# Optimization experiments

Measured on AMD Instinct MI355X. Metric: run time of the kernel, lower is better.

The kernel has to match this reference:

```python
import jax, jax.numpy as jnp
from jax import lax
import numpy as np

NA, NC = 3, 1
CONF_THRESH, IOU_THRESH = 0.5, 0.5


def _conv(x, w, b, pad):
    y = lax.conv_general_dilated(x, w, (1, 1), [(pad, pad), (pad, pad)],
                                 dimension_numbers=('NCHW', 'OIHW', 'NCHW'))
    return y + b[None, :, None, None]


def _maxpool2(x):
    return lax.reduce_window(x, -jnp.inf, lax.max, (1, 1, 2, 2), (1, 1, 2, 2), 'VALID')


def _stream(x, w1, b1, w2, b2):
    x = _maxpool2(jax.nn.relu(_conv(x, w1, b1, 1)))
    x = _maxpool2(jax.nn.relu(_conv(x, w2, b2, 1)))
    return x


def _pairwise_iou(b):
    # b: [N,4] in (x1,y1,x2,y2); matches torchvision box_iou (no area clamp)
    x1, y1, x2, y2 = b[:, 0], b[:, 1], b[:, 2], b[:, 3]
    area = (x2 - x1) * (y2 - y1)
    ix1 = jnp.maximum(x1[:, None], x1[None, :])
    iy1 = jnp.maximum(y1[:, None], y1[None, :])
    ix2 = jnp.minimum(x2[:, None], x2[None, :])
    iy2 = jnp.minimum(y2[:, None], y2[None, :])
    inter = jnp.clip(ix2 - ix1, 0.0) * jnp.clip(iy2 - iy1, 0.0)
    return inter / (area[:, None] + area[None, :] - inter)


def _nms_keep(boxes, scores, conf_keep, iou_thresh):
    # Greedy NMS over a fixed, small N; returns bool keep mask (conf + NMS).
    n = boxes.shape[0]
    order = jnp.argsort(-jnp.where(conf_keep, scores, -jnp.inf))
    iou = _pairwise_iou(boxes[order])  # [N,N] in score order
    idx = jnp.arange(n)

    def body(i, state):
        keep, suppressed = state
        valid = jnp.logical_not(suppressed[i])
        keep = keep.at[i].set(valid)
        suppressed = suppressed | (valid & (iou[i] > iou_thresh) & (idx > i))
        return keep, suppressed

    keep_sorted, _ = lax.fori_loop(0, n, body,
                                   (jnp.zeros(n, bool), jnp.zeros(n, bool)))
    keep = jnp.zeros(n, bool).at[order].set(keep_sorted)
    return keep & conf_keep


def setup_inputs() -> dict:
    key = jax.random.key(0)
    ks = jax.random.split(key, 14)
    s = 0.05
    inp = {
        'x': jax.random.normal(ks[0], (8, 3, 512, 512), jnp.float32),
        'rgb_w1': jax.random.normal(ks[1], (32, 3, 3, 3), jnp.float32) * s,
        'rgb_b1': jnp.zeros((32,), jnp.float32),
        'rgb_w2': jax.random.normal(ks[2], (64, 32, 3, 3), jnp.float32) * s,
        'rgb_b2': jnp.zeros((64,), jnp.float32),
        'ir_w1': jax.random.normal(ks[3], (32, 3, 3, 3), jnp.float32) * s,
        'ir_b1': jnp.zeros((32,), jnp.float32),
        'ir_w2': jax.random.normal(ks[4], (64, 32, 3, 3), jnp.float32) * s,
        'ir_b2': jnp.zeros((64,), jnp.float32),
        'fuse_w': jax.random.normal(ks[5], (128, 128, 3, 3), jnp.float32) * s,
        'fuse_b': jnp.zeros((128,), jnp.float32),
        'det_w': jax.random.normal(ks[6], (NA * (5 + NC), 128, 1, 1), jnp.float32),
        'det_b': jax.random.normal(ks[7], (NA * (5 + NC),), jnp.float32),
    }
    return inp


def reference(x, rgb_w1, rgb_b1, rgb_w2, rgb_b2,
              ir_w1, ir_b1, ir_w2, ir_b2,
              fuse_w, fuse_b, det_w, det_b):
    f1 = _stream(x, rgb_w1, rgb_b1, rgb_w2, rgb_b2)   # [B,64,H/4,W/4]
    f2 = _stream(x, ir_w1, ir_b1, ir_w2, ir_b2)       # [B,64,H/4,W/4]
    f = jnp.concatenate([f1, f2], axis=1)             # [B,128,H/4,W/4]
    f = jax.nn.relu(_conv(f, fuse_w, fuse_b, 1))
    f = jnp.mean(f, axis=(2, 3), keepdims=True)       # AdaptiveAvgPool2d((1,1))
    p = _conv(f, det_w, det_b, 0)                     # [B,18,1,1]
    B, C, H, W = p.shape
    p = p.reshape(B, NA, 5 + NC, H, W).transpose(0, 1, 3, 4, 2)  # [B,na,H,W,5+nc]
    boxes = p[..., :4].reshape(B, -1, 4)              # [B, na*H*W, 4]
    scores = jax.nn.sigmoid(p[..., 4]).reshape(B, -1) # [B, na*H*W]
    conf_keep = scores > CONF_THRESH
    keep = jax.vmap(_nms_keep, in_axes=(0, 0, 0, None))(boxes, scores, conf_keep,
                                                        IOU_THRESH)
    # Fixed-shape equivalent of the per-image variable-length preds list:
    # preds[b] == boxes[b][keep[b]].
    return p, boxes, scores, keep
```

## Files before the change

kernel.cpp:

```cpp
#include <hip/hip_runtime.h>
#include <math.h>


typedef __bf16 bf16x8 __attribute__((ext_vector_type(8)));
typedef float f32x4 __attribute__((ext_vector_type(4)));

static __device__ __forceinline__ ushort f2bf(float f) {
    unsigned u = __float_as_uint(f);
    unsigned r = (u + 0x7fffu + ((u >> 16) & 1u)) >> 16;
    return (ushort)r;
}
static __device__ __forceinline__ float bf2f(ushort h) {
    return __uint_as_float(((unsigned)h) << 16);
}
static __device__ __forceinline__ void gl_lds16(const void* g, void* l) {
    __builtin_amdgcn_global_load_lds(
        (const __attribute__((address_space(1))) void*)g,
        (__attribute__((address_space(3))) void*)l, 16, 0, 0);
}

__global__ __launch_bounds__(256) void w1prep(
    const float* __restrict__ w_rgb, const float* __restrict__ w_ir,
    uint* __restrict__ W1p)
{
    int i = blockIdx.x * 256 + threadIdx.x;
    if (i >= 2048) return;
    int s = i >> 10, r = i & 1023;
    int oc = r >> 5, k = r & 31;
    const float* w = s ? w_ir : w_rgb;
    float v = (k < 27) ? w[oc * 27 + k] : 0.f;
    ushort h = f2bf(v);
    W1p[i] = (uint)h | ((uint)f2bf(v - bf2f(h)) << 16);
}

__global__ __launch_bounds__(256) void conv1_mfma(
    const float* __restrict__ x, const uint* __restrict__ W1p,
    const float* __restrict__ bias, ushort* __restrict__ C1h,
    ushort* __restrict__ C1l)
{
    __shared__ uint S[3 * 4 * 132];
    __shared__ float pool[4][32][32];

    const int seg = blockIdx.x, Y = blockIdx.y, b = blockIdx.z;
    const int tid = threadIdx.x, wsub = tid >> 6, lane = tid & 63;
    const int n = lane & 15, q = lane >> 4;

    uint4 bu0a = *(const uint4*)&W1p[n * 32 + q * 8];
    uint4 bu0b = *(const uint4*)&W1p[n * 32 + q * 8 + 4];
    uint4 bu1a = *(const uint4*)&W1p[(16 + n) * 32 + q * 8];
    uint4 bu1b = *(const uint4*)&W1p[(16 + n) * 32 + q * 8 + 4];

    const int ih0 = 2 * Y - 1, iw0 = seg * 128 - 1;
    for (int i = tid; i < 1584; i += 256) {
        int c = i / 528, rem = i - c * 528;
        int r = rem / 132, cc = rem - r * 132;
        int ih = ih0 + r, iw = iw0 + cc;
        float v = 0.f;
        if (cc < 130 && ih >= 0 && ih < 512 && iw >= 0 && iw < 512)
            v = x[((b * 3 + c) * 512 + ih) * 512 + iw];
        ushort h = f2bf(v);
        S[i] = (uint)h | ((uint)f2bf(v - bf2f(h)) << 16);
    }

    uint4 bh0v, bl0v, bh1v, bl1v;
    {
        uint u0[8], u1[8];
        *(uint4*)&u0[0] = bu0a; *(uint4*)&u0[4] = bu0b;
        *(uint4*)&u1[0] = bu1a; *(uint4*)&u1[4] = bu1b;
        uint* bh0 = (uint*)&bh0v; uint* bl0 = (uint*)&bl0v;
        uint* bh1 = (uint*)&bh1v; uint* bl1 = (uint*)&bl1v;
#pragma unroll
        for (int j = 0; j < 4; ++j) {
            bh0[j] = (u0[2 * j] & 0xffffu) | (u0[2 * j + 1] << 16);
            bl0[j] = (u0[2 * j] >> 16) | (u0[2 * j + 1] & 0xffff0000u);
            bh1[j] = (u1[2 * j] & 0xffffu) | (u1[2 * j + 1] << 16);
            bl1[j] = (u1[2 * j] >> 16) | (u1[2 * j + 1] & 0xffff0000u);
        }
    }
    bf16x8 Bh0 = __builtin_bit_cast(bf16x8, bh0v);
    bf16x8 Bl0 = __builtin_bit_cast(bf16x8, bl0v);
    bf16x8 Bh1 = __builtin_bit_cast(bf16x8, bh1v);
    bf16x8 Bl1 = __builtin_bit_cast(bf16x8, bl1v);

    int idx[8];
    const int off0 = (wsub & 1) * 132 + (wsub >> 1) * 64 + n;
#pragma unroll
    for (int e = 0; e < 8; ++e) {
        int k = q * 8 + e;
        int c = (k >= 18) ? ((k >= 27) ? 3 : 2) : ((k >= 9) ? 1 : 0);
        int t = k - c * 9;
        int ky = (t >= 6) ? 2 : ((t >= 3) ? 1 : 0);
        int kx = t - ky * 3;
        idx[e] = (k < 27) ? ((c * 4 + ky) * 132 + kx + off0) : 0;
    }
    __syncthreads();

    f32x4 acc[4][2];
#pragma unroll
    for (int mt = 0; mt < 4; ++mt)
#pragma unroll
        for (int nt = 0; nt < 2; ++nt) acc[mt][nt] = (f32x4){0.f, 0.f, 0.f, 0.f};

#pragma unroll
    for (int mt = 0; mt < 4; ++mt) {
        uint u[8];
#pragma unroll
        for (int e = 0; e < 8; ++e) u[e] = S[idx[e] + mt * 16];
        uint4 ahv, alv;
        uint* ah = (uint*)&ahv;
        uint* al = (uint*)&alv;
#pragma unroll
        for (int j = 0; j < 4; ++j) {
            ah[j] = (u[2 * j] & 0xffffu) | (u[2 * j + 1] << 16);
            al[j] = (u[2 * j] >> 16) | (u[2 * j + 1] & 0xffff0000u);
        }
        bf16x8 Ah = __builtin_bit_cast(bf16x8, ahv);
        bf16x8 Al = __builtin_bit_cast(bf16x8, alv);
        __builtin_amdgcn_s_setprio(1);
        acc[mt][0] = __builtin_amdgcn_mfma_f32_16x16x32_bf16(Ah, Bh0, acc[mt][0], 0, 0, 0);
        acc[mt][1] = __builtin_amdgcn_mfma_f32_16x16x32_bf16(Ah, Bh1, acc[mt][1], 0, 0, 0);
        acc[mt][0] = __builtin_amdgcn_mfma_f32_16x16x32_bf16(Ah, Bl0, acc[mt][0], 0, 0, 0);
        acc[mt][1] = __builtin_amdgcn_mfma_f32_16x16x32_bf16(Ah, Bl1, acc[mt][1], 0, 0, 0);
        acc[mt][0] = __builtin_amdgcn_mfma_f32_16x16x32_bf16(Al, Bh0, acc[mt][0], 0, 0, 0);
        acc[mt][1] = __builtin_amdgcn_mfma_f32_16x16x32_bf16(Al, Bh1, acc[mt][1], 0, 0, 0);
        __builtin_amdgcn_s_setprio(0);
    }

#pragma unroll
    for (int mt = 0; mt < 4; ++mt)
#pragma unroll
        for (int nt = 0; nt < 2; ++nt) {
            int oc = nt * 16 + n;
            int plx = mt * 8 + q * 2;
            pool[wsub][plx][oc]     = fmaxf(acc[mt][nt][0], acc[mt][nt][1]);
            pool[wsub][plx + 1][oc] = fmaxf(acc[mt][nt][2], acc[mt][nt][3]);
        }
    __syncthreads();
    {
        int plx = tid >> 2, ocq = tid & 3;
        int wp = plx >> 5, pl = plx & 31;
        __attribute__((aligned(16))) ushort hb[8], lb[8];
#pragma unroll
        for (int e = 0; e < 8; ++e) {
            int oc = ocq * 8 + e;
            float v = fmaxf(pool[wp * 2][pl][oc], pool[wp * 2 + 1][pl][oc]);
            v = fmaxf(v + bias[oc], 0.f);
            ushort h = f2bf(v);
            hb[e] = h;
            lb[e] = f2bf(v - bf2f(h));
        }
        int ow = seg * 64 + plx;
        size_t base = (((size_t)((b * 256 + Y) * 256 + ow)) << 5) + ocq * 8;
        *(uint4*)(C1h + base) = *(const uint4*)hb;
        *(uint4*)(C1l + base) = *(const uint4*)lb;
    }
}

__global__ __launch_bounds__(256) void conv2_mfma(
    const ushort* __restrict__ C1h, const ushort* __restrict__ C1l,
    const float* __restrict__ w2, const float* __restrict__ bias,
    ushort* __restrict__ Ahi, ushort* __restrict__ Alo, int stream_base)
{
    __shared__ __attribute__((aligned(16))) char lds[58368];
    ushort* BhL = (ushort*)(lds + 33792);
    ushort* BlL = (ushort*)(lds + 46080);
    float (*pool)[32][64] = (float (*)[32][64])lds;

    const int seg = blockIdx.x, Y = blockIdx.y, b = blockIdx.z;
    const int tid = threadIdx.x, wsub = tid >> 6, lane = tid & 63;
    const int n = lane & 15, q = lane >> 4;
    const int rs = wsub & 1;
    const int xs = wsub >> 1;

    const uint4 zero4 = make_uint4(0u, 0u, 0u, 0u);

    f32x4 acc[4][4];
#pragma unroll
    for (int mt = 0; mt < 4; ++mt)
#pragma unroll
        for (int nt = 0; nt < 4; ++nt) acc[mt][nt] = (f32x4){0.f, 0.f, 0.f, 0.f};

    for (int ky = 0; ky < 3; ++ky) {
        if (ky) __syncthreads();

        {
            const int hl = wsub >> 1, rsS = wsub & 1;
            const int yy = 2 * Y + rsS + ky - 1;
            char* dstbase = lds + hl * 16896 + rsS * 8448 + 64;
            if (yy >= 0 && yy < 256) {
                const ushort* src = (hl ? C1l : C1h)
                    + ((size_t)(b * 256 + yy) * 256 + seg * 128) * 32;
                const char* s8 = (const char*)src + lane * 16;
#pragma unroll
                for (int j = 0; j < 8; ++j)
                    gl_lds16(s8 + j * 1024, dstbase + j * 1024);
            } else {
#pragma unroll
                for (int j = 0; j < 8; ++j)
                    *(uint4*)(dstbase + j * 1024 + lane * 16) = zero4;
            }
        }
        if (tid < 32) {
            int combo = tid >> 3;
            int hl = combo >> 1, rsE = combo & 1;
            int e = (tid >> 2) & 1, part = tid & 3;
            int yy = 2 * Y + rsE + ky - 1;
            int xp = seg * 128 + (e ? 128 : -1);
            uint4 v = zero4;
            if (yy >= 0 && yy < 256 && xp >= 0 && xp < 256) {
                const ushort* src = (hl ? C1l : C1h)
                    + ((size_t)(b * 256 + yy) * 256 + xp) * 32 + part * 8;
                v = *(const uint4*)src;
            }
            *(uint4*)(lds + hl * 16896 + rsE * 8448 + (e ? 129 * 64 : 0) + part * 16) = v;
        }
        for (int i = tid; i < 6144; i += 256) {
            int t = ky * 3 + (i >> 11), r = i & 2047;
            float v = w2[r * 9 + t];
            ushort h = f2bf(v);
            BhL[i] = h;
            BlL[i] = f2bf(v - bf2f(h));
        }
        __syncthreads();

        for (int kx = 0; kx < 3; ++kx) {
            uint4 cH[4], cL[4];
#pragma unroll
            for (int mt = 0; mt < 4; ++mt) {
                int off = rs * 8448 + (xs * 64 + mt * 16 + n + kx) * 64 + q * 16;
                cH[mt] = *(const uint4*)(lds + off);
                cL[mt] = *(const uint4*)(lds + 16896 + off);
            }
            bf16x8 bh[4], bl[4];
#pragma unroll
            for (int nt = 0; nt < 4; ++nt) {
                int off = kx * 2048 + (nt * 16 + n) * 32 + q * 8;
                bh[nt] = __builtin_bit_cast(bf16x8, *(const uint4*)&BhL[off]);
                bl[nt] = __builtin_bit_cast(bf16x8, *(const uint4*)&BlL[off]);
            }
            __builtin_amdgcn_s_setprio(1);
#pragma unroll
            for (int mt = 0; mt < 4; ++mt) {
                bf16x8 ah = __builtin_bit_cast(bf16x8, cH[mt]);
#pragma unroll
                for (int nt = 0; nt < 4; ++nt)
                    acc[mt][nt] = __builtin_amdgcn_mfma_f32_16x16x32_bf16(ah, bh[nt], acc[mt][nt], 0, 0, 0);
            }
#pragma unroll
            for (int mt = 0; mt < 4; ++mt) {
                bf16x8 ah = __builtin_bit_cast(bf16x8, cH[mt]);
#pragma unroll
                for (int nt = 0; nt < 4; ++nt)
                    acc[mt][nt] = __builtin_amdgcn_mfma_f32_16x16x32_bf16(ah, bl[nt], acc[mt][nt], 0, 0, 0);
            }
#pragma unroll
            for (int mt = 0; mt < 4; ++mt) {
                bf16x8 al = __builtin_bit_cast(bf16x8, cL[mt]);
#pragma unroll
                for (int nt = 0; nt < 4; ++nt)
                    acc[mt][nt] = __builtin_amdgcn_mfma_f32_16x16x32_bf16(al, bh[nt], acc[mt][nt], 0, 0, 0);
            }
            __builtin_amdgcn_s_setprio(0);
        }
    }

    __syncthreads();

#pragma unroll
    for (int mt = 0; mt < 4; ++mt)
#pragma unroll
        for (int nt = 0; nt < 4; ++nt) {
            int oc = nt * 16 + n;
            int plx = mt * 8 + q * 2;
            pool[wsub][plx][oc]     = fmaxf(acc[mt][nt][0], acc[mt][nt][1]);
            pool[wsub][plx + 1][oc] = fmaxf(acc[mt][nt][2], acc[mt][nt][3]);
        }
    __syncthreads();

    {
        int plx = tid >> 2, ocq = tid & 3;
        int wp = plx >> 5, pl = plx & 31;
        __attribute__((aligned(16))) ushort hb[16], lb[16];
#pragma unroll
        for (int e = 0; e < 16; ++e) {
            int oc = ocq * 16 + e;
            float v = fmaxf(pool[wp * 2][pl][oc], pool[wp * 2 + 1][pl][oc]);
            v = fmaxf(v + bias[oc], 0.f);
            ushort h = f2bf(v);
            hb[e] = h;
            lb[e] = f2bf(v - bf2f(h));
        }
        int gx = seg * 64 + plx;
        int cpl = (stream_base >> 5) + (ocq >> 1);
        int cho = (ocq & 1) * 16;
        size_t base = (((size_t)(((b * 4 + cpl) * 128 + Y) * 128 + gx)) << 5) + cho;
        uint4* dh = (uint4*)(Ahi + base);
        uint4* dl = (uint4*)(Alo + base);
        dh[0] = *(const uint4*)&hb[0];
        dh[1] = *(const uint4*)&hb[8];
        dl[0] = *(const uint4*)&lb[0];
        dl[1] = *(const uint4*)&lb[8];
    }
}

__global__ __launch_bounds__(256) void wprep(
    const float* __restrict__ fw, ushort* __restrict__ Whi,
    ushort* __restrict__ Wlo)
{
    int idx = blockIdx.x * 256 + threadIdx.x;
    if (idx >= 147456) return;
    int kk = idx & 31;
    int oc = (idx >> 5) & 127;
    int ct = idx >> 12;
    int c = ct / 9, t = ct - c * 9;
    int ic = c * 32 + kk;
    int ky = t / 3, kx = t - ky * 3;
    float v = fw[((oc * 128 + ic) * 3 + ky) * 3 + kx];
    ushort h = f2bf(v);
    Whi[idx] = h;
    Wlo[idx] = f2bf(v - bf2f(h));
}

__global__ __launch_bounds__(256, 2) void fuse_mfma(
    const ushort* __restrict__ Ahi, const ushort* __restrict__ Alo,
    const ushort* __restrict__ Whi, const ushort* __restrict__ Wlo,
    const float* __restrict__ bias, float* __restrict__ featsum)
{
    __shared__ float partial[4][128];
    const int b = blockIdx.x, ypair = blockIdx.y;
    const int tid = threadIdx.x, wsub = tid >> 6, lane = tid & 63;
    const int n = lane & 15, q = lane >> 4;
    const int y = ypair * 2 + (wsub >> 1);
    const int xbase = (wsub & 1) * 64;

    f32x4 acc[4][8];
#pragma unroll
    for (int mt = 0; mt < 4; ++mt)
#pragma unroll
        for (int g = 0; g < 8; ++g) acc[mt][g] = (f32x4){0.f, 0.f, 0.f, 0.f};

    const uint4 zero4 = make_uint4(0u, 0u, 0u, 0u);

    auto loadA = [&](int tc, uint4* oh, uint4* ol) {
        int c = tc / 9, t = tc - c * 9;
        int ky = t / 3, kx = t - ky * 3;
        int yy = y + ky - 1;
        bool yok = (yy >= 0) & (yy < 128);
#pragma unroll
        for (int mt = 0; mt < 4; ++mt) {
            int xp = xbase + mt * 16 + n + kx - 1;
            bool ok = yok & (xp >= 0) & (xp < 128);
            int yyc = ok ? yy : 0, xpc = ok ? xp : 0;
            size_t aoff = (((size_t)(((b * 4 + c) * 128 + yyc) * 128 + xpc)) << 5) + q * 8;
            oh[mt] = ok ? *(const uint4*)(Ahi + aoff) : zero4;
            ol[mt] = ok ? *(const uint4*)(Alo + aoff) : zero4;
        }
    };

    uint4 pAh[4], pAl[4];
    loadA(0, pAh, pAl);

    const ushort* WhiB = Whi + n * 32 + q * 8;
    const ushort* WloB = Wlo + n * 32 + q * 8;

    uint4 nBh[4], nBl[4];
#pragma unroll
    for (int j = 0; j < 4; ++j) {
        nBh[j] = *(const uint4*)(WhiB + j * 512);
        nBl[j] = *(const uint4*)(WloB + j * 512);
    }

    for (int tc = 0; tc < 36; ++tc) {
        uint4 cAh[4], cAl[4];
#pragma unroll
        for (int mt = 0; mt < 4; ++mt) { cAh[mt] = pAh[mt]; cAl[mt] = pAl[mt]; }
        if (tc + 1 < 36) loadA(tc + 1, pAh, pAl);
#pragma unroll
        for (int g = 0; g < 8; ++g) {
            const int slot = g & 3;
            bf16x8 bh = __builtin_bit_cast(bf16x8, nBh[slot]);
            bf16x8 bl = __builtin_bit_cast(bf16x8, nBl[slot]);
            {
                size_t off = (size_t)(tc * 8 + g + 4) * 512;
                nBh[slot] = *(const uint4*)(WhiB + off);
                nBl[slot] = *(const uint4*)(WloB + off);
            }
#pragma unroll
            for (int mt = 0; mt < 4; ++mt) {
                bf16x8 ah = __builtin_bit_cast(bf16x8, cAh[mt]);
                acc[mt][g] = __builtin_amdgcn_mfma_f32_16x16x32_bf16(ah, bh, acc[mt][g], 0, 0, 0);
            }
#pragma unroll
            for (int mt = 0; mt < 4; ++mt) {
                bf16x8 ah = __builtin_bit_cast(bf16x8, cAh[mt]);
                acc[mt][g] = __builtin_amdgcn_mfma_f32_16x16x32_bf16(ah, bl, acc[mt][g], 0, 0, 0);
            }
#pragma unroll
            for (int mt = 0; mt < 4; ++mt) {
                bf16x8 al = __builtin_bit_cast(bf16x8, cAl[mt]);
                acc[mt][g] = __builtin_amdgcn_mfma_f32_16x16x32_bf16(al, bh, acc[mt][g], 0, 0, 0);
            }
        }
    }

#pragma unroll
    for (int g = 0; g < 8; ++g) {
        float bv = bias[g * 16 + n];
        float v = 0.f;
#pragma unroll
        for (int mt = 0; mt < 4; ++mt)
#pragma unroll
            for (int r = 0; r < 4; ++r) v += fmaxf(acc[mt][g][r] + bv, 0.f);
        v += __shfl_xor(v, 16);
        v += __shfl_xor(v, 32);
        if (lane < 16) partial[wsub][g * 16 + lane] = v;
    }
    __syncthreads();
    if (tid < 128) {
        float v = partial[0][tid] + partial[1][tid] + partial[2][tid] + partial[3][tid];
        atomicAdd(&featsum[b * 128 + tid], v);
    }
}

__global__ void det_nms(const float* __restrict__ featsum,
                        const float* __restrict__ dw, const float* __restrict__ db,
                        float* __restrict__ out)
{
    const int b = threadIdx.x;
    if (b >= 8) return;
    const float inv = 1.0f / 16384.0f;

    float p[18];
    for (int j = 0; j < 18; ++j) {
        float a = db[j];
        const float* wp = &dw[j * 128];
        const float* f = &featsum[b * 128];
        for (int c = 0; c < 128; ++c) a = fmaf(wp[c], f[c] * inv, a);
        p[j] = a;
    }
    for (int a = 0; a < 3; ++a)
        for (int e = 0; e < 6; ++e) out[b * 18 + a * 6 + e] = p[a * 6 + e];

    float bx[3][4], sc[3];
    bool ck[3];
    for (int a = 0; a < 3; ++a) {
        for (int k = 0; k < 4; ++k) {
            bx[a][k] = p[a * 6 + k];
            out[144 + b * 12 + a * 4 + k] = bx[a][k];
        }
        float sg = 1.f / (1.f + expf(-p[a * 6 + 4]));
        sc[a] = sg;
        ck[a] = sg > 0.5f;
        out[240 + b * 3 + a] = sg;
    }

    float key[3];
    int order[3];
    bool used[3] = {false, false, false};
    for (int a = 0; a < 3; ++a) key[a] = ck[a] ? sc[a] : -INFINITY;
    for (int i = 0; i < 3; ++i) {
        int best = -1;
        float bk = 0.f;
        for (int a = 0; a < 3; ++a) {
            if (used[a]) continue;
            if (best < 0 || key[a] > bk) { best = a; bk = key[a]; }
        }
        order[i] = best;
        used[best] = true;
    }

    float X1[3], Y1[3], X2[3], Y2[3], AR[3];
    for (int i = 0; i < 3; ++i) {
        int o = order[i];
        X1[i] = bx[o][0]; Y1[i] = bx[o][1];
        X2[i] = bx[o][2]; Y2[i] = bx[o][3];
        AR[i] = (X2[i] - X1[i]) * (Y2[i] - Y1[i]);
    }
    bool suppressed[3] = {false, false, false}, keep_s[3];
    for (int i = 0; i < 3; ++i) {
        bool valid = !suppressed[i];
        keep_s[i] = valid;
        if (valid) {
            for (int j = i + 1; j < 3; ++j) {
                float ix1 = fmaxf(X1[i], X1[j]), iy1 = fmaxf(Y1[i], Y1[j]);
                float ix2 = fminf(X2[i], X2[j]), iy2 = fminf(Y2[i], Y2[j]);
                float inter = fmaxf(ix2 - ix1, 0.f) * fmaxf(iy2 - iy1, 0.f);
                float iou = inter / (AR[i] + AR[j] - inter);
                if (iou > 0.5f) suppressed[j] = true;
            }
        }
    }
    bool keep[3];
    for (int i = 0; i < 3; ++i) keep[order[i]] = keep_s[i];
    for (int a = 0; a < 3; ++a)
        out[264 + b * 3 + a] = (keep[a] && ck[a]) ? 1.f : 0.f;
}

__global__ void zero_feat(float* __restrict__ p)
{
    int i = blockIdx.x * 256 + threadIdx.x;
    if (i < 1024) p[i] = 0.f;
}

extern "C" void kernel_launch(void* const* d_in, const int* in_sizes, int n_in,
                              void* d_out, int out_size, void* d_ws, size_t ws_size,
                              hipStream_t stream)
{
    const float* x      = (const float*)d_in[0];
    const float* rgb_w1 = (const float*)d_in[1];
    const float* rgb_b1 = (const float*)d_in[2];
    const float* rgb_w2 = (const float*)d_in[3];
    const float* rgb_b2 = (const float*)d_in[4];
    const float* ir_w1  = (const float*)d_in[5];
    const float* ir_b1  = (const float*)d_in[6];
    const float* ir_w2  = (const float*)d_in[7];
    const float* ir_b2  = (const float*)d_in[8];
    const float* fuse_w = (const float*)d_in[9];
    const float* fuse_b = (const float*)d_in[10];
    const float* det_w  = (const float*)d_in[11];
    const float* det_b  = (const float*)d_in[12];
    float* out = (float*)d_out;

    char* ws = (char*)d_ws;
    ushort* C1h  = (ushort*)(ws);
    ushort* C1l  = (ushort*)(ws + 33554432);
    ushort* Whi  = (ushort*)(ws);
    ushort* Wlo  = (ushort*)(ws + 299008);
    float*  feat = (float*)(ws + 598016);
    ushort* Ahi  = (ushort*)(ws + 67108864);
    ushort* Alo  = (ushort*)(ws + 100663296);
    uint*   W1p  = (uint*)(ws + 134209536);

    dim3 blk(256);
    hipLaunchKernelGGL(w1prep, dim3(8), blk, 0, stream, rgb_w1, ir_w1, W1p);
    hipLaunchKernelGGL(conv1_mfma, dim3(4, 256, 8), blk, 0, stream, x, W1p, rgb_b1, C1h, C1l);
    hipLaunchKernelGGL(conv2_mfma, dim3(2, 128, 8), blk, 0, stream, C1h, C1l, rgb_w2, rgb_b2, Ahi, Alo, 0);
    hipLaunchKernelGGL(conv1_mfma, dim3(4, 256, 8), blk, 0, stream, x, W1p + 1024, ir_b1, C1h, C1l);
    hipLaunchKernelGGL(conv2_mfma, dim3(2, 128, 8), blk, 0, stream, C1h, C1l, ir_w2, ir_b2, Ahi, Alo, 64);
    hipLaunchKernelGGL(wprep, dim3(576), blk, 0, stream, fuse_w, Whi, Wlo);
    hipLaunchKernelGGL(zero_feat, dim3(4), blk, 0, stream, feat);
    hipLaunchKernelGGL(fuse_mfma, dim3(8, 64), blk, 0, stream, Ahi, Alo, Whi, Wlo, fuse_b, feat);
    hipLaunchKernelGGL(det_nms, dim3(1), dim3(64), 0, stream, feat, det_w, det_b, out);
}
```

Before: 494.8 us.

## Stage fuse-conv activations and weights in LDS; pad pool arrays against bank conflicts

The fuse convolution kernel now copies one input row (hi/lo bf16) and three kx weight slices per (channel chunk, ky) into LDS using global_load_lds, then reads both from LDS for all three kx taps. Previously each wave loaded A and B directly from global memory. The work is split so each block handles one output row, with waves divided across x-halves and output-channel halves, which doubles the grid. The pool scratch arrays in conv1 and conv2 also get one padding column to reduce LDS bank conflicts. In exchange, 64KB of LDS lowers occupancy and adds barriers each iteration.

```diff
diff --git a/kernel.cpp b/kernel.cpp
--- a/kernel.cpp
+++ b/kernel.cpp
@@ -39,7 +39,7 @@
     ushort* __restrict__ C1l)
 {
     __shared__ uint S[3 * 4 * 132];
-    __shared__ float pool[4][32][32];
+    __shared__ float pool[4][32][33];
 
     const int seg = blockIdx.x, Y = blockIdx.y, b = blockIdx.z;
     const int tid = threadIdx.x, wsub = tid >> 6, lane = tid & 63;
@@ -164,7 +164,7 @@
     __shared__ __attribute__((aligned(16))) char lds[58368];
     ushort* BhL = (ushort*)(lds + 33792);
     ushort* BlL = (ushort*)(lds + 46080);
-    float (*pool)[32][64] = (float (*)[32][64])lds;
+    float (*pool)[32][65] = (float (*)[32][65])lds;
 
     const int seg = blockIdx.x, Y = blockIdx.y, b = blockIdx.z;
     const int tid = threadIdx.x, wsub = tid >> 6, lane = tid & 63;
@@ -326,86 +326,106 @@
     const ushort* __restrict__ Whi, const ushort* __restrict__ Wlo,
     const float* __restrict__ bias, float* __restrict__ featsum)
 {
-    __shared__ float partial[4][128];
-    const int b = blockIdx.x, ypair = blockIdx.y;
+    __shared__ __attribute__((aligned(16))) char lds[65536];
+
+    const int b = blockIdx.x, y = blockIdx.y;
     const int tid = threadIdx.x, wsub = tid >> 6, lane = tid & 63;
     const int n = lane & 15, q = lane >> 4;
-    const int y = ypair * 2 + (wsub >> 1);
-    const int xbase = (wsub & 1) * 64;
-
-    f32x4 acc[4][8];
+    const int p = wsub & 1, o = wsub >> 1;
+
+    const uint4 zero4 = make_uint4(0u, 0u, 0u, 0u);
+    const bool badL = (p == 0) & (n == 0);
+    const bool badR = (p == 1) & (n == 15);
+
+    f32x4 acc[4][4];
 #pragma unroll
     for (int mt = 0; mt < 4; ++mt)
 #pragma unroll
-        for (int g = 0; g < 8; ++g) acc[mt][g] = (f32x4){0.f, 0.f, 0.f, 0.f};
-
-    const uint4 zero4 = make_uint4(0u, 0u, 0u, 0u);
-
-    auto loadA = [&](int tc, uint4* oh, uint4* ol) {
-        int c = tc / 9, t = tc - c * 9;
-        int ky = t / 3, kx = t - ky * 3;
-        int yy = y + ky - 1;
-        bool yok = (yy >= 0) & (yy < 128);
-#pragma unroll
-        for (int mt = 0; mt < 4; ++mt) {
-            int xp = xbase + mt * 16 + n + kx - 1;
-            bool ok = yok & (xp >= 0) & (xp < 128);
-            int yyc = ok ? yy : 0, xpc = ok ? xp : 0;
-            size_t aoff = (((size_t)(((b * 4 + c) * 128 + yyc) * 128 + xpc)) << 5) + q * 8;
-            oh[mt] = ok ? *(const uint4*)(Ahi + aoff) : zero4;
-            ol[mt] = ok ? *(const uint4*)(Alo + aoff) : zero4;
-        }
-    };
-
-    uint4 pAh[4], pAl[4];
-    loadA(0, pAh, pAl);
-
-    const ushort* WhiB = Whi + n * 32 + q * 8;
-    const ushort* WloB = Wlo + n * 32 + q * 8;
-
-    uint4 nBh[4], nBl[4];
-#pragma unroll
-    for (int j = 0; j < 4; ++j) {
-        nBh[j] = *(const uint4*)(WhiB + j * 512);
-        nBl[j] = *(const uint4*)(WloB + j * 512);
-    }
-
-    for (int tc = 0; tc < 36; ++tc) {
-        uint4 cAh[4], cAl[4];
-#pragma unroll
-        for (int mt = 0; mt < 4; ++mt) { cAh[mt] = pAh[mt]; cAl[mt] = pAl[mt]; }
-        if (tc + 1 < 36) loadA(tc + 1, pAh, pAl);
-#pragma unroll
-        for (int g = 0; g < 8; ++g) {
-            const int slot = g & 3;
-            bf16x8 bh = __builtin_bit_cast(bf16x8, nBh[slot]);
-            bf16x8 bl = __builtin_bit_cast(bf16x8, nBl[slot]);
-            {
-                size_t off = (size_t)(tc * 8 + g + 4) * 512;
-                nBh[slot] = *(const uint4*)(WhiB + off);
-                nBl[slot] = *(const uint4*)(WloB + off);
-            }
-#pragma unroll
-            for (int mt = 0; mt < 4; ++mt) {
-                bf16x8 ah = __builtin_bit_cast(bf16x8, cAh[mt]);
-                acc[mt][g] = __builtin_amdgcn_mfma_f32_16x16x32_bf16(ah, bh, acc[mt][g], 0, 0, 0);
-            }
-#pragma unroll
-            for (int mt = 0; mt < 4; ++mt) {
-                bf16x8 ah = __builtin_bit_cast(bf16x8, cAh[mt]);
-                acc[mt][g] = __builtin_amdgcn_mfma_f32_16x16x32_bf16(ah, bl, acc[mt][g], 0, 0, 0);
-            }
-#pragma unroll
-            for (int mt = 0; mt < 4; ++mt) {
-                bf16x8 al = __builtin_bit_cast(bf16x8, cAl[mt]);
-                acc[mt][g] = __builtin_amdgcn_mfma_f32_16x16x32_bf16(al, bh, acc[mt][g], 0, 0, 0);
-            }
-        }
-    }
-
-#pragma unroll
-    for (int g = 0; g < 8; ++g) {
-        float bv = bias[g * 16 + n];
+        for (int g = 0; g < 4; ++g) acc[mt][g] = (f32x4){0.f, 0.f, 0.f, 0.f};
+
+    for (int c = 0; c < 4; ++c) {
+        for (int ky = 0; ky < 3; ++ky) {
+            if (c | ky) __syncthreads();
+
+            if (wsub == 0) {
+                const int yy = y + ky - 1;
+                if (yy >= 0 && yy < 128) {
+                    const char* sH = (const char*)(Ahi + ((size_t)((b * 4 + c) * 128 + yy)) * 4096) + lane * 16;
+                    const char* sL = (const char*)(Alo + ((size_t)((b * 4 + c) * 128 + yy)) * 4096) + lane * 16;
+#pragma unroll
+                    for (int j = 0; j < 8; ++j) {
+                        gl_lds16(sH + j * 1024, lds + j * 1024);
+                        gl_lds16(sL + j * 1024, lds + 8192 + j * 1024);
+                    }
+                } else {
+#pragma unroll
+                    for (int j = 0; j < 16; ++j)
+                        *(uint4*)(lds + j * 1024 + lane * 16) = zero4;
+                }
+            } else {
+                const size_t woff = (size_t)(c * 9 + ky * 3) * 4096;
+                const int bc0 = (wsub - 1) * 16;
+#pragma unroll
+                for (int j = 0; j < 16; ++j) {
+                    int bc = bc0 + j;
+                    const ushort* base = (bc < 24) ? (Whi + woff) : (Wlo + woff);
+                    int co = (bc < 24) ? bc : (bc - 24);
+                    gl_lds16((const char*)base + co * 1024 + lane * 16,
+                             lds + 16384 + bc * 1024);
+                }
+            }
+            __syncthreads();
+
+#pragma unroll
+            for (int kx = 0; kx < 3; ++kx) {
+                bf16x8 bh[4], bl[4];
+#pragma unroll
+                for (int g = 0; g < 4; ++g) {
+                    int boff = 16384 + kx * 8192 + (o * 64 + g * 16 + n) * 64 + q * 16;
+                    bh[g] = __builtin_bit_cast(bf16x8, *(const uint4*)(lds + boff));
+                    bl[g] = __builtin_bit_cast(bf16x8, *(const uint4*)(lds + boff + 24576));
+                }
+                uint4 cH[4], cL[4];
+#pragma unroll
+                for (int mt = 0; mt < 4; ++mt) {
+                    int s = p * 64 + mt * 16 + n + kx - 1;
+                    if (kx == 0 && mt == 0) s = (s < 0) ? 0 : s;
+                    if (kx == 2 && mt == 3) s = (s > 127) ? 127 : s;
+                    int aoff = s * 64 + q * 16;
+                    cH[mt] = *(const uint4*)(lds + aoff);
+                    cL[mt] = *(const uint4*)(lds + 8192 + aoff);
+                }
+                if (kx == 0) { cH[0] = badL ? zero4 : cH[0]; cL[0] = badL ? zero4 : cL[0]; }
+                if (kx == 2) { cH[3] = badR ? zero4 : cH[3]; cL[3] = badR ? zero4 : cL[3]; }
+
+#pragma unroll
+                for (int g = 0; g < 4; ++g) {
+#pragma unroll
+                    for (int mt = 0; mt < 4; ++mt) {
+                        bf16x8 ah = __builtin_bit_cast(bf16x8, cH[mt]);
+                        acc[mt][g] = __builtin_amdgcn_mfma_f32_16x16x32_bf16(ah, bh[g], acc[mt][g], 0, 0, 0);
+                    }
+#pragma unroll
+                    for (int mt = 0; mt < 4; ++mt) {
+                        bf16x8 ah = __builtin_bit_cast(bf16x8, cH[mt]);
+                        acc[mt][g] = __builtin_amdgcn_mfma_f32_16x16x32_bf16(ah, bl[g], acc[mt][g], 0, 0, 0);
+                    }
+#pragma unroll
+                    for (int mt = 0; mt < 4; ++mt) {
+                        bf16x8 al = __builtin_bit_cast(bf16x8, cL[mt]);
+                        acc[mt][g] = __builtin_amdgcn_mfma_f32_16x16x32_bf16(al, bh[g], acc[mt][g], 0, 0, 0);
+                    }
+                }
+            }
+        }
+    }
+
+    __syncthreads();
+    float* partial = (float*)lds;
+
+#pragma unroll
+    for (int g = 0; g < 4; ++g) {
+        float bv = bias[o * 64 + g * 16 + n];
         float v = 0.f;
 #pragma unroll
         for (int mt = 0; mt < 4; ++mt)
@@ -413,13 +433,11 @@
             for (int r = 0; r < 4; ++r) v += fmaxf(acc[mt][g][r] + bv, 0.f);
         v += __shfl_xor(v, 16);
         v += __shfl_xor(v, 32);
-        if (lane < 16) partial[wsub][g * 16 + lane] = v;
+        if (lane < 16) partial[p * 128 + o * 64 + g * 16 + lane] = v;
     }
     __syncthreads();
-    if (tid < 128) {
-        float v = partial[0][tid] + partial[1][tid] + partial[2][tid] + partial[3][tid];
-        atomicAdd(&featsum[b * 128 + tid], v);
-    }
+    if (tid < 128)
+        atomicAdd(&featsum[b * 128 + tid], partial[tid] + partial[128 + tid]);
 }
 
 __global__ void det_nms(const float* __restrict__ featsum,
@@ -539,6 +557,6 @@
     hipLaunchKernelGGL(conv2_mfma, dim3(2, 128, 8), blk, 0, stream, C1h, C1l, ir_w2, ir_b2, Ahi, Alo, 64);
     hipLaunchKernelGGL(wprep, dim3(576), blk, 0, stream, fuse_w, Whi, Wlo);
     hipLaunchKernelGGL(zero_feat, dim3(4), blk, 0, stream, feat);
-    hipLaunchKernelGGL(fuse_mfma, dim3(8, 64), blk, 0, stream, Ahi, Alo, Whi, Wlo, fuse_b, feat);
+    hipLaunchKernelGGL(fuse_mfma, dim3(8, 128), blk, 0, stream, Ahi, Alo, Whi, Wlo, fuse_b, feat);
     hipLaunchKernelGGL(det_nms, dim3(1), dim3(64), 0, stream, feat, det_w, det_b, out);
 }
```

New measurement: 701.0 us. +41.7%, slower.
